# Kernel optimization log

Measured on AMD Instinct MI355X. Metric: run time of the kernel, lower is better.

The kernel has to match this reference:

```python
import jax, jax.numpy as jnp
import numpy as np

N = 100000
B = 1024
NODE_DIM = 128
LATENT = 128
IN_DIM = NODE_DIM + 2 * LATENT   # 384, q/kv projection input width
FFN_IN = LATENT + IN_DIM          # 512, ffn input width


def setup_inputs() -> dict:
    key = jax.random.key(0)
    ks = jax.random.split(key, 16)
    s = 1.0 / np.sqrt(IN_DIM)
    s2 = 1.0 / np.sqrt(FFN_IN)
    s3 = 1.0 / np.sqrt(LATENT)
    return {
        "x": jax.random.normal(ks[0], (N, NODE_DIM), jnp.float32),
        "memory": jax.random.normal(ks[1], (N, LATENT), jnp.float32),
        "delta_t_vec": jax.random.normal(ks[2], (N, LATENT), jnp.float32),
        "tar_t_vec": jax.random.normal(ks[3], (B, LATENT), jnp.float32),
        # sparse neighbor mask, ~50 neighbors per target on average
        "neighbor_mask": jax.random.uniform(ks[4], (B, N)) < 5e-4,
        "tar_idx": jax.random.randint(ks[5], (B, 1), 0, N, jnp.int32),
        "Wq": jax.random.uniform(ks[6], (LATENT, IN_DIM), jnp.float32, -s, s),
        "bq": jnp.zeros((LATENT,), jnp.float32),
        "Wk": jax.random.uniform(ks[7], (LATENT, IN_DIM), jnp.float32, -s, s),
        "bk": jnp.zeros((LATENT,), jnp.float32),
        "Wv": jax.random.uniform(ks[8], (LATENT, IN_DIM), jnp.float32, -s, s),
        "bv": jnp.zeros((LATENT,), jnp.float32),
        "W1": jax.random.uniform(ks[9], (LATENT, FFN_IN), jnp.float32, -s2, s2),
        "b1": jnp.zeros((LATENT,), jnp.float32),
        "W2": jax.random.uniform(ks[10], (LATENT, LATENT), jnp.float32, -s3, s3),
        "b2": jnp.zeros((LATENT,), jnp.float32),
    }


def reference(x, memory, delta_t_vec, tar_t_vec, neighbor_mask, tar_idx,
              Wq, bq, Wk, bk, Wv, bv, W1, b1, W2, b2):
    idx = tar_idx[:, 0]                                  # [B]
    q_input = jnp.concatenate([x[idx], memory[idx], tar_t_vec], axis=-1)   # [B, IN_DIM]
    kv_input = jnp.concatenate([x, memory, delta_t_vec], axis=-1)          # [N, IN_DIM]
    q = q_input @ Wq.T + bq                              # [B, D]
    k = kv_input @ Wk.T + bk                             # [N, D]
    v = kv_input @ Wv.T + bv                             # [N, D]
    d = q.shape[-1]
    scores = jnp.einsum("bd,nd->bn", q, k) / jnp.sqrt(jnp.float32(d))      # [B, N]
    # rows with no neighbors attend to their own target node
    no_neighbor = ~jnp.any(neighbor_mask, axis=1)        # [B]
    self_mask = jnp.arange(neighbor_mask.shape[1])[None, :] == tar_idx     # [B, N]
    mask = neighbor_mask | (no_neighbor[:, None] & self_mask)
    scores = jnp.where(mask, scores, -jnp.inf)
    attn = jax.nn.softmax(scores, axis=-1)               # [B, N]
    agg = attn @ v                                       # [B, D]
    z = jnp.concatenate([agg, q_input], axis=-1)         # [B, FFN_IN]
    z = jax.nn.relu(z @ W1.T + b1) @ W2.T + b2           # [B, D]
    return z
```

## Files before the change

kernel.cpp:

```cpp
#include <hip/hip_runtime.h>
#include <stdint.h>
#include <stddef.h>

constexpr int N_NODES = 100000;
constexpr int BATCH   = 1024;
constexpr int LAT     = 128;
constexpr int INDIM   = 384;
constexpr int FFNIN   = 512;
constexpr int NB_MAX  = 512;

__global__ __launch_bounds__(384) void fused_graph_attn_kernel(
    const float* __restrict__ x,   const float* __restrict__ mem,
    const float* __restrict__ dtv, const float* __restrict__ ttv,
    const uint32_t* __restrict__ mask, const int* __restrict__ tar_idx,
    const float* __restrict__ Wq, const float* __restrict__ bq,
    const float* __restrict__ Wk, const float* __restrict__ bk,
    const float* __restrict__ Wv, const float* __restrict__ bv,
    const float* __restrict__ W1, const float* __restrict__ b1,
    const float* __restrict__ W2, const float* __restrict__ b2,
    float* __restrict__ out)
{
    const int b    = blockIdx.x;
    const int tid  = threadIdx.x;
    const int lane = tid & 63;
    const int wave = tid >> 6;

    __shared__ int   cnt;
    __shared__ int   jl[NB_MAX];
    __shared__ float sc[NB_MAX];
    __shared__ float qin[INDIM];
    __shared__ float qv[LAT];
    __shared__ float qk[INDIM];
    __shared__ float u[INDIM];
    __shared__ float zbuf[FFNIN];
    __shared__ float hbuf[LAT];
    __shared__ float sbias_sh;

    const int idx = tar_idx[b];
    if (tid == 0) cnt = 0;

    if (tid < 128)      qin[tid] = x[(size_t)idx * LAT + tid];
    else if (tid < 256) qin[tid] = mem[(size_t)idx * LAT + (tid - 128)];
    else                qin[tid] = ttv[(size_t)b * LAT + (tid - 256)];
    __syncthreads();

    {
        const uint4* row = (const uint4*)(mask + (size_t)b * N_NODES);
        for (int i = tid; i < N_NODES / 4; i += 384) {
            uint4 v = row[i];
            if (v.x | v.y | v.z | v.w) {
                uint32_t w[4] = {v.x, v.y, v.z, v.w};
                #pragma unroll
                for (int wi = 0; wi < 4; ++wi) {
                    if (w[wi]) {
                        int slot = atomicAdd(&cnt, 1);
                        if (slot < NB_MAX) jl[slot] = i * 4 + wi;
                    }
                }
            }
        }
    }
    __syncthreads();
    if (tid == 0 && cnt == 0) { jl[0] = idx; cnt = 1; }
    __syncthreads();
    const int nb = cnt < NB_MAX ? cnt : NB_MAX;

    if (tid < LAT) {
        const float4* wr = (const float4*)(Wq + (size_t)tid * INDIM);
        float acc = bq[tid];
        #pragma unroll 4
        for (int i = 0; i < INDIM / 4; ++i) {
            float4 w = wr[i];
            acc += w.x * qin[4*i] + w.y * qin[4*i+1] + w.z * qin[4*i+2] + w.w * qin[4*i+3];
        }
        qv[tid] = acc;
    }
    __syncthreads();

    {
        float acc = 0.f;
        #pragma unroll 8
        for (int d = 0; d < LAT; ++d) acc += qv[d] * Wk[(size_t)d * INDIM + tid];
        qk[tid] = acc;
    }
    if (wave == 0) {
        float p = qv[lane] * bk[lane] + qv[lane + 64] * bk[lane + 64];
        for (int off = 32; off; off >>= 1) p += __shfl_down(p, off, 64);
        if (lane == 0) sbias_sh = p;
    }
    __syncthreads();

    const float scale = 0.088388347648318447f;
    const float sb = sbias_sh;
    for (int jj = wave; jj < nb; jj += 6) {
        int j = jl[jj];
        const float* xp = x   + (size_t)j * LAT;
        const float* mp = mem + (size_t)j * LAT;
        const float* dp = dtv + (size_t)j * LAT;
        float p = qk[lane]       * xp[lane] + qk[lane + 64]  * xp[lane + 64]
                + qk[128 + lane] * mp[lane] + qk[192 + lane] * mp[lane + 64]
                + qk[256 + lane] * dp[lane] + qk[320 + lane] * dp[lane + 64];
        for (int off = 32; off; off >>= 1) p += __shfl_down(p, off, 64);
        if (lane == 0) sc[jj] = (p + sb) * scale;
    }
    __syncthreads();

    if (wave == 0) {
        float m = -INFINITY;
        for (int t = lane; t < nb; t += 64) m = fmaxf(m, sc[t]);
        for (int off = 32; off; off >>= 1) m = fmaxf(m, __shfl_down(m, off, 64));
        m = __shfl(m, 0, 64);
        float s = 0.f;
        for (int t = lane; t < nb; t += 64) { float e = __expf(sc[t] - m); sc[t] = e; s += e; }
        for (int off = 32; off; off >>= 1) s += __shfl_down(s, off, 64);
        s = __shfl(s, 0, 64);
        float inv = 1.f / s;
        for (int t = lane; t < nb; t += 64) sc[t] *= inv;
    }
    __syncthreads();

    {
        const float* src = (tid < 128) ? x : (tid < 256 ? mem : dtv);
        const int off128 = tid & 127;
        float acc = 0.f;
        for (int jj = 0; jj < nb; ++jj)
            acc += sc[jj] * src[(size_t)jl[jj] * LAT + off128];
        u[tid] = acc;
    }
    __syncthreads();

    if (tid < LAT) {
        const float4* wr = (const float4*)(Wv + (size_t)tid * INDIM);
        float acc = bv[tid];
        #pragma unroll 4
        for (int i = 0; i < INDIM / 4; ++i) {
            float4 w = wr[i];
            acc += w.x * u[4*i] + w.y * u[4*i+1] + w.z * u[4*i+2] + w.w * u[4*i+3];
        }
        zbuf[tid] = acc;
    }
    zbuf[LAT + tid] = qin[tid];
    __syncthreads();

    if (tid < LAT) {
        const float4* wr = (const float4*)(W1 + (size_t)tid * FFNIN);
        float acc = b1[tid];
        #pragma unroll 4
        for (int i = 0; i < FFNIN / 4; ++i) {
            float4 w = wr[i];
            acc += w.x * zbuf[4*i] + w.y * zbuf[4*i+1] + w.z * zbuf[4*i+2] + w.w * zbuf[4*i+3];
        }
        hbuf[tid] = fmaxf(acc, 0.f);
    }
    __syncthreads();

    if (tid < LAT) {
        const float4* wr = (const float4*)(W2 + (size_t)tid * LAT);
        float acc = b2[tid];
        #pragma unroll 4
        for (int i = 0; i < LAT / 4; ++i) {
            float4 w = wr[i];
            acc += w.x * hbuf[4*i] + w.y * hbuf[4*i+1] + w.z * hbuf[4*i+2] + w.w * hbuf[4*i+3];
        }
        out[(size_t)b * LAT + tid] = acc;
    }
}

extern "C" void kernel_launch(void* const* d_in, const int* in_sizes, int n_in,
                              void* d_out, int out_size, void* d_ws, size_t ws_size,
                              hipStream_t stream) {
    const float*    x    = (const float*)d_in[0];
    const float*    mem  = (const float*)d_in[1];
    const float*    dtv  = (const float*)d_in[2];
    const float*    ttv  = (const float*)d_in[3];
    const uint32_t* mask = (const uint32_t*)d_in[4];
    const int*      tidx = (const int*)d_in[5];
    const float*    Wq   = (const float*)d_in[6];
    const float*    bq   = (const float*)d_in[7];
    const float*    Wk   = (const float*)d_in[8];
    const float*    bk   = (const float*)d_in[9];
    const float*    Wv   = (const float*)d_in[10];
    const float*    bv   = (const float*)d_in[11];
    const float*    W1   = (const float*)d_in[12];
    const float*    b1   = (const float*)d_in[13];
    const float*    W2   = (const float*)d_in[14];
    const float*    b2   = (const float*)d_in[15];
    float* out = (float*)d_out;

    fused_graph_attn_kernel<<<BATCH, 384, 0, stream>>>(
        x, mem, dtv, ttv, mask, tidx, Wq, bq, Wk, bk, Wv, bv, W1, b1, W2, b2,
        out);
}
```

Measured before the change: 710.8 us.

## Warp-specialize the mask scan and compute the q projection concurrently on a spare wave

Five waves now scan the neighbor mask row with nontemporal vector loads. Meanwhile the sixth wave gathers the query input, computes the Wq projection, the Wk-folded query vector and the bias term. This overlaps the projection work with the memory-bound mask scan and removes a barrier. The cost is that the scan runs with fewer waves, and the q projection is serialized onto a single wave, which could become the critical path if the scan finishes early.

```diff
diff --git a/kernel.cpp b/kernel.cpp
--- a/kernel.cpp
+++ b/kernel.cpp
@@ -8,6 +8,8 @@
 constexpr int INDIM   = 384;
 constexpr int FFNIN   = 512;
 constexpr int NB_MAX  = 512;
+
+typedef unsigned int uint4v __attribute__((ext_vector_type(4)));
 
 __global__ __launch_bounds__(384) void fused_graph_attn_kernel(
     const float* __restrict__ x,   const float* __restrict__ mem,
@@ -38,16 +40,12 @@
 
     const int idx = tar_idx[b];
     if (tid == 0) cnt = 0;
-
-    if (tid < 128)      qin[tid] = x[(size_t)idx * LAT + tid];
-    else if (tid < 256) qin[tid] = mem[(size_t)idx * LAT + (tid - 128)];
-    else                qin[tid] = ttv[(size_t)b * LAT + (tid - 256)];
-    __syncthreads();
-
-    {
-        const uint4* row = (const uint4*)(mask + (size_t)b * N_NODES);
-        for (int i = tid; i < N_NODES / 4; i += 384) {
-            uint4 v = row[i];
+    __syncthreads();
+
+    if (wave < 5) {
+        const uint4v* row = (const uint4v*)(mask + (size_t)b * N_NODES);
+        for (int i = tid; i < N_NODES / 4; i += 320) {
+            uint4v v = __builtin_nontemporal_load(&row[i]);
             if (v.x | v.y | v.z | v.w) {
                 uint32_t w[4] = {v.x, v.y, v.z, v.w};
                 #pragma unroll
@@ -59,36 +57,57 @@
                 }
             }
         }
+    } else {
+        qin[lane]       = x[(size_t)idx * LAT + lane];
+        qin[lane + 64]  = x[(size_t)idx * LAT + lane + 64];
+        qin[lane + 128] = mem[(size_t)idx * LAT + lane];
+        qin[lane + 192] = mem[(size_t)idx * LAT + lane + 64];
+        qin[lane + 256] = ttv[(size_t)b * LAT + lane];
+        qin[lane + 320] = ttv[(size_t)b * LAT + lane + 64];
+
+        #pragma unroll
+        for (int h = 0; h < 2; ++h) {
+            const int o = lane + 64 * h;
+            const float4* wr = (const float4*)(Wq + (size_t)o * INDIM);
+            float acc = bq[o];
+            #pragma unroll 4
+            for (int i = 0; i < INDIM / 4; ++i) {
+                float4 w = wr[i];
+                acc += w.x * qin[4*i] + w.y * qin[4*i+1] + w.z * qin[4*i+2] + w.w * qin[4*i+3];
+            }
+            qv[o] = acc;
+        }
+
+        {
+            float acc0 = 0.f, acc1 = 0.f, acc2 = 0.f, acc3 = 0.f, acc4 = 0.f, acc5 = 0.f;
+            for (int d = 0; d < LAT; ++d) {
+                const float qd = qv[d];
+                const float* wk = Wk + (size_t)d * INDIM + lane;
+                acc0 += qd * wk[0];
+                acc1 += qd * wk[64];
+                acc2 += qd * wk[128];
+                acc3 += qd * wk[192];
+                acc4 += qd * wk[256];
+                acc5 += qd * wk[320];
+            }
+            qk[lane]       = acc0;
+            qk[lane + 64]  = acc1;
+            qk[lane + 128] = acc2;
+            qk[lane + 192] = acc3;
+            qk[lane + 256] = acc4;
+            qk[lane + 320] = acc5;
+        }
+
+        {
+            float p = qv[lane] * bk[lane] + qv[lane + 64] * bk[lane + 64];
+            for (int off = 32; off; off >>= 1) p += __shfl_down(p, off, 64);
+            if (lane == 0) sbias_sh = p;
+        }
     }
     __syncthreads();
     if (tid == 0 && cnt == 0) { jl[0] = idx; cnt = 1; }
     __syncthreads();
     const int nb = cnt < NB_MAX ? cnt : NB_MAX;
-
-    if (tid < LAT) {
-        const float4* wr = (const float4*)(Wq + (size_t)tid * INDIM);
-        float acc = bq[tid];
-        #pragma unroll 4
-        for (int i = 0; i < INDIM / 4; ++i) {
-            float4 w = wr[i];
-            acc += w.x * qin[4*i] + w.y * qin[4*i+1] + w.z * qin[4*i+2] + w.w * qin[4*i+3];
-        }
-        qv[tid] = acc;
-    }
-    __syncthreads();
-
-    {
-        float acc = 0.f;
-        #pragma unroll 8
-        for (int d = 0; d < LAT; ++d) acc += qv[d] * Wk[(size_t)d * INDIM + tid];
-        qk[tid] = acc;
-    }
-    if (wave == 0) {
-        float p = qv[lane] * bk[lane] + qv[lane + 64] * bk[lane + 64];
-        for (int off = 32; off; off >>= 1) p += __shfl_down(p, off, 64);
-        if (lane == 0) sbias_sh = p;
-    }
-    __syncthreads();
 
     const float scale = 0.088388347648318447f;
     const float sb = sbias_sh;
```

Measured after the change: 721.7 us. Within noise of the previous version (+1.5%).
